# Performance work log

Hardware: AMD Instinct MI355X
Metric: run time of the kernel (lower is better)

## Reference

```python
import jax, jax.numpy as jnp
import numpy as np

T, N = 64, 512
DL, DA, DV = 300, 128, 128
HL, HA, HV = 256, 128, 128
MEM, DF = 256, 128
H_ATT1, H_ATT2, H_G1, H_G2, H_OUT = 512, 512, 512, 512, 256
BETA, M_MOD = 2.0, 3
ATT_IN = (HL + HA + HV) * 2      # cStar dim (windowsize=2)
G_IN = ATT_IN + MEM


def setup_inputs() -> dict:
    key = jax.random.key(0)
    ks = iter(jax.random.split(key, 48))

    def p(*shape):
        return jax.random.normal(next(ks), shape, jnp.float32) * 0.05

    inp = {}
    inp["x"] = jax.random.normal(next(ks), (T, N, DL + DA + DV), jnp.float32)
    for m, (d, h) in (("l", (DL, HL)), ("a", (DA, HA)), ("v", (DV, HV))):
        inp["Wih_" + m] = p(4 * h, d)   # torch LSTMCell weight_ih [4h, d]
        inp["Whh_" + m] = p(4 * h, h)
        inp["bih_" + m] = p(4 * h)
        inp["bhh_" + m] = p(4 * h)
    inp["att1_w1"], inp["att1_b1"] = p(H_ATT1, ATT_IN), p(H_ATT1)
    inp["att1_w2"], inp["att1_b2"] = p(ATT_IN, H_ATT1), p(ATT_IN)
    inp["att2_w1"], inp["att2_b1"] = p(H_ATT2, ATT_IN), p(H_ATT2)
    inp["att2_w2"], inp["att2_b2"] = p(MEM, H_ATT2), p(MEM)
    inp["g1_w1"], inp["g1_b1"] = p(H_G1, G_IN), p(H_G1)
    inp["g1_w2"], inp["g1_b2"] = p(MEM, H_G1), p(MEM)
    inp["g2_w1"], inp["g2_b1"] = p(H_G2, G_IN), p(H_G2)
    inp["g2_w2"], inp["g2_b2"] = p(MEM, H_G2), p(MEM)
    inp["fl_w"], inp["fl_b"] = p(DF, HL), p(DF)
    inp["fa_w"], inp["fa_b"] = p(DF, HA), p(DF)
    inp["fv_w"], inp["fv_b"] = p(DF, HV), p(DF)
    inp["o_w1"], inp["o_b1"] = p(H_OUT, DF + MEM), p(H_OUT)
    inp["o_w2"], inp["o_b2"] = p(1, H_OUT), p(1)
    return inp


def _lin(z, w, b):
    return z @ w.T + b


def _lstm_cell(xt, h, c, Wih, Whh, bih, bhh):
    # torch.nn.LSTMCell: gate order i, f, g, o
    gates = xt @ Wih.T + h @ Whh.T + bih + bhh
    i, f, g, o = jnp.split(gates, 4, axis=1)
    c2 = jax.nn.sigmoid(f) * c + jax.nn.sigmoid(i) * jnp.tanh(g)
    h2 = jax.nn.sigmoid(o) * jnp.tanh(c2)
    return h2, c2


def reference(x, Wih_l, Whh_l, bih_l, bhh_l, Wih_a, Whh_a, bih_a, bhh_a,
              Wih_v, Whh_v, bih_v, bhh_v,
              att1_w1, att1_b1, att1_w2, att1_b2,
              att2_w1, att2_b1, att2_w2, att2_b2,
              g1_w1, g1_b1, g1_w2, g1_b2, g2_w1, g2_b1, g2_w2, g2_b2,
              fl_w, fl_b, fa_w, fa_b, fv_w, fv_b,
              o_w1, o_b1, o_w2, o_b2):
    n = x.shape[1]

    def step(carry, xt):
        h_l, c_l, h_a, c_a, h_v, c_v, mem = carry
        x_l, x_a, x_v = xt[:, :DL], xt[:, DL:DL + DA], xt[:, DL + DA:]
        nh_l, nc_l = _lstm_cell(x_l, h_l, c_l, Wih_l, Whh_l, bih_l, bhh_l)
        nh_a, nc_a = _lstm_cell(x_a, h_a, c_a, Wih_a, Whh_a, bih_a, bhh_a)
        nh_v, nc_v = _lstm_cell(x_v, h_v, c_v, Wih_v, Whh_v, bih_v, bhh_v)
        # cStar = [prev cells, new cells]  -> [n, ATT_IN]
        cStar = jnp.concatenate([c_l, c_a, c_v, nc_l, nc_a, nc_v], axis=1)
        att = jax.nn.softmax(
            _lin(jax.nn.relu(_lin(cStar, att1_w1, att1_b1)), att1_w2, att1_b2),
            axis=1)
        attended = att * cStar
        cHat = jnp.tanh(
            _lin(jax.nn.relu(_lin(attended, att2_w1, att2_b1)), att2_w2, att2_b2))
        both = jnp.concatenate([attended, mem], axis=1)
        gamma1 = jax.nn.sigmoid(
            _lin(jax.nn.relu(_lin(both, g1_w1, g1_b1)), g1_w2, g1_b2))
        gamma2 = jax.nn.sigmoid(
            _lin(jax.nn.relu(_lin(both, g2_w1, g2_b1)), g2_w2, g2_b2))
        mem = gamma1 * mem + gamma2 * cHat
        return (nh_l, nc_l, nh_a, nc_a, nh_v, nc_v, mem), None

    z = lambda d: jnp.zeros((n, d), x.dtype)
    init = (z(HL), z(HL), z(HA), z(HA), z(HV), z(HV), z(MEM))
    (h_l, c_l, h_a, c_a, h_v, c_v, mem), _ = jax.lax.scan(step, init, x)

    def compute_exp(logits):
        return jnp.exp(logits - jnp.max(logits))  # global max, as in source

    p_l = compute_exp(_lin(h_l, fl_w, fl_b))
    p_a = compute_exp(_lin(h_a, fa_w, fa_b))
    p_v = compute_exp(_lin(h_v, fv_w, fv_b))
    e = BETA / (M_MOD - 1)
    lav = (p_l ** e) * jnp.log(p_l) + (p_a ** e) * jnp.log(p_a) + (p_v ** e) * jnp.log(p_v)
    last_hs = jnp.concatenate([lav, mem], axis=1)
    out = _lin(jax.nn.relu(_lin(last_hs, o_w1, o_b1)), o_w2, o_b2)
    return out.flatten()
```

## Files before the change

kernel.cpp:

```cpp
#include <hip/hip_runtime.h>
#include <string.h>

typedef __bf16 bf16_t;
typedef bf16_t bf16x8 __attribute__((ext_vector_type(8)));
typedef bf16_t bf16x4 __attribute__((ext_vector_type(4)));
typedef float  f32x4  __attribute__((ext_vector_type(4)));

#define MFMA16(a,b,c) __builtin_amdgcn_mfma_f32_16x16x32_bf16((a),(b),(c),0,0,0)

#define TSTEPS 64
#define NB     512
#define DIN    556
#define LDSK   40
#define GRIDP  256
#define GXD    33

#define HWREG_XCC_ID (20 | (0 << 6) | ((4 - 1) << 11))

#define OFF_WIHP_L 0u
#define OFF_WHH_L  327680u
#define OFF_WIHP_A 589824u
#define OFF_WHH_A  655360u
#define OFF_WIHP_V 720896u
#define OFF_WHH_V  786432u
#define OFF_ATT1W1 851968u
#define OFF_ATT1W2 1376256u
#define OFF_ATT2W1 1900544u
#define OFF_ATT2W2 2424832u
#define OFF_G1W1   2555904u
#define OFF_G1W2   3211264u
#define OFF_G2W1   3342336u
#define OFF_G2W2   3997696u
#define OFF_FLW    4128768u
#define OFF_FAW    4161536u
#define OFF_FVW    4177920u

__device__ __forceinline__ float sigmoidf_(float x) {
  return 1.0f / (1.0f + __expf(-x));
}
__device__ __forceinline__ float tanhf_(float x) {
  x = fminf(fmaxf(x, -15.0f), 15.0f);
  float e = __expf(2.0f * x);
  return (e - 1.0f) / (e + 1.0f);
}

struct PArgs {
  const float* x;
  const float* bih_l; const float* bhh_l;
  const float* bih_a; const float* bhh_a;
  const float* bih_v; const float* bhh_v;
  const float* att1_b1; const float* att1_b2;
  const float* att2_b1; const float* att2_b2;
  const float* g1_b1; const float* g1_b2;
  const float* g2_b1; const float* g2_b2;
  const float* fl_b; const float* fa_b; const float* fv_b;
  const float* o_w1; const float* o_b1; const float* o_w2; const float* o_b2;
  const float* cvt_src[17];
  unsigned cvt_dst[17];
  int cvt_K[17]; int cvt_Kpad[17]; int cvt_rows[17];
  bf16_t* POOL; bf16_t* XL; bf16_t* XA; bf16_t* XV;
  bf16_t* HB0; bf16_t* HB1; float* CBUF; float* MEMF; bf16_t* MEMBF;
  bf16_t* CSTAR; bf16_t* CSTAR2; bf16_t* Z1; float* LOGB; bf16_t* ATTD; bf16_t* Z3;
  float* PL; float* MAXP; float* BSUM;
  unsigned* BAR;
  float* out;
  int allow_team;
};


__device__ __forceinline__ void gbar(unsigned* bar, unsigned k, int bid) {
  __syncthreads();
  if (threadIdx.x == 0) {
    __threadfence();
    unsigned* gc   = bar + (bid & 7) * 16;
    unsigned* root = bar + 128;
    if (__hip_atomic_fetch_add(gc, 1u, __ATOMIC_ACQ_REL, __HIP_MEMORY_SCOPE_AGENT)
        == 32u * (k + 1u) - 1u) {
      __hip_atomic_fetch_add(root, 1u, __ATOMIC_ACQ_REL, __HIP_MEMORY_SCOPE_AGENT);
    }
    while (__hip_atomic_load(root, __ATOMIC_RELAXED, __HIP_MEMORY_SCOPE_AGENT)
           < 8u * (k + 1u)) {
      __builtin_amdgcn_s_sleep(1);
    }
    __threadfence();
  }
  __syncthreads();
}

__device__ __forceinline__ void lbar(unsigned* ctr, unsigned target) {
  asm volatile("s_waitcnt vmcnt(0)" ::: "memory");
  __syncthreads();
  if (threadIdx.x == 0) {
    __hip_atomic_fetch_add(ctr, 1u, __ATOMIC_RELAXED, __HIP_MEMORY_SCOPE_AGENT);
    while (__hip_atomic_load(ctr, __ATOMIC_RELAXED, __HIP_MEMORY_SCOPE_AGENT)
           < target) {
      __builtin_amdgcn_s_sleep(1);
    }
    asm volatile("buffer_inv\n\ts_waitcnt vmcnt(0)" ::: "memory");
  }
  __syncthreads();
}

__device__ __forceinline__ void gates_body(const PArgs& p, int job, int t, char* SM,
                                           const bf16_t* hbase, bf16_t* houtb,
                                           bf16_t* cstar)
{
  bf16_t* AlB[2] = { (bf16_t*)SM,            (bf16_t*)(SM + 5120) };
  bf16_t* WlB[2] = { (bf16_t*)(SM + 10240),  (bf16_t*)(SM + 20480) };
  float (*Gx)[64][GXD] = (float (*)[64][GXD])SM;

  const int tid = threadIdx.x;
  const int m0 = (job >> 4) * 64;
  const int y  = job & 15;

  const bf16_t *xp, *Wih, *Whh;
  int Kx, Hm, hoff, j0, oldbase, boff;
  if (y < 8) {
    xp = p.XL + (size_t)t * NB * 320; Wih = p.POOL + OFF_WIHP_L; Whh = p.POOL + OFF_WHH_L;
    Kx = 320; Hm = 256; hoff = 0; j0 = y * 32; oldbase = 0; boff = 0;
  } else if (y < 12) {
    xp = p.XA + (size_t)t * NB * 128; Wih = p.POOL + OFF_WIHP_A; Whh = p.POOL + OFF_WHH_A;
    Kx = 128; Hm = 128; hoff = 131072; j0 = (y - 8) * 32; oldbase = 256; boff = 1024;
  } else {
    xp = p.XV + (size_t)t * NB * 128; Wih = p.POOL + OFF_WIHP_V; Whh = p.POOL + OFF_WHH_V;
    Kx = 128; Hm = 128; hoff = 196608; j0 = (y - 12) * 32; oldbase = 384; boff = 1536;
  }

  const int wave = tid >> 6, lane = tid & 63;
  const int lrow = lane & 15, quad = lane >> 4;
  const int srow = tid >> 2, schunk = (tid & 3) * 8;
  const int wrow = tid >> 1, wchunk = (tid & 1) * 16;
  const int g = wrow >> 5, jr = wrow & 31;

  f32x4 acc[4][2];
  #pragma unroll
  for (int mi = 0; mi < 4; mi++)
    #pragma unroll
    for (int ni = 0; ni < 2; ni++) acc[mi][ni] = f32x4{0.f, 0.f, 0.f, 0.f};

  for (int ph = 0; ph < 2; ph++) {
    const bf16_t* Ab; const bf16_t* Wb; int lda_, ldw_, K_;
    if (ph == 0) { Ab = xp;            lda_ = Kx; K_ = Kx; Wb = Wih; ldw_ = Kx; }
    else         { Ab = hbase + hoff;  lda_ = Hm; K_ = Hm; Wb = Whh; ldw_ = Hm; }

    const bf16_t* Arow = Ab + (size_t)(m0 + srow) * lda_ + schunk;
    const bf16_t* Wrow = Wb + (size_t)(g * Hm + j0 + jr) * ldw_ + wchunk;
    const int nI = K_ >> 5;

    bf16x8 av  = *(const bf16x8*)(Arow);
    bf16x8 wv0 = *(const bf16x8*)(Wrow);
    bf16x8 wv1 = *(const bf16x8*)(Wrow + 8);
    *(bf16x8*)(AlB[0] + srow * LDSK + schunk) = av;
    *(bf16x8*)(WlB[0] + wrow * LDSK + wchunk) = wv0;
    *(bf16x8*)(WlB[0] + wrow * LDSK + wchunk + 8) = wv1;

    for (int i = 0; i < nI; i++) {
      const int cur = i & 1;
      const bool more = (i + 1 < nI);
      if (more) {
        av  = *(const bf16x8*)(Arow + (i + 1) * 32);
        wv0 = *(const bf16x8*)(Wrow + (i + 1) * 32);
        wv1 = *(const bf16x8*)(Wrow + (i + 1) * 32 + 8);
      }
      __syncthreads();
      if (more) {
        *(bf16x8*)(AlB[cur ^ 1] + srow * LDSK + schunk) = av;
        *(bf16x8*)(WlB[cur ^ 1] + wrow * LDSK + wchunk) = wv0;
        *(bf16x8*)(WlB[cur ^ 1] + wrow * LDSK + wchunk + 8) = wv1;
      }
      bf16x8 afr[4], bfr[2];
      #pragma unroll
      for (int mi = 0; mi < 4; mi++)
        afr[mi] = *(const bf16x8*)(AlB[cur] + (mi * 16 + lrow) * LDSK + quad * 8);
      #pragma unroll
      for (int ni = 0; ni < 2; ni++)
        bfr[ni] = *(const bf16x8*)(WlB[cur] + (wave * 32 + ni * 16 + lrow) * LDSK + quad * 8);
      #pragma unroll
      for (int mi = 0; mi < 4; mi++)
        #pragma unroll
        for (int ni = 0; ni < 2; ni++)
          acc[mi][ni] = MFMA16(afr[mi], bfr[ni], acc[mi][ni]);
    }
    __syncthreads();
  }

  #pragma unroll
  for (int mi = 0; mi < 4; mi++)
    #pragma unroll
    for (int ni = 0; ni < 2; ni++) {
      int col = ni * 16 + lrow;
      float bv = p.BSUM[boff + wave * Hm + j0 + col];
      #pragma unroll
      for (int r = 0; r < 4; r++) {
        Gx[wave][mi * 16 + quad * 4 + r][col] = acc[mi][ni][r] + bv;
      }
    }
  __syncthreads();

  float* cbuf = p.CBUF + hoff;
  int m = tid >> 2, jb = (tid & 3) * 8;
  #pragma unroll
  for (int i = 0; i < 8; i++) {
    int j = jb + i;
    float gi = Gx[0][m][j], gf = Gx[1][m][j], gg = Gx[2][m][j], go = Gx[3][m][j];
    size_t off = (size_t)(m0 + m) * Hm + (j0 + j);
    float c_old = cbuf[off];
    float c2 = sigmoidf_(gf) * c_old + sigmoidf_(gi) * tanhf_(gg);
    float h2 = sigmoidf_(go) * tanhf_(c2);
    cbuf[off] = c2;
    houtb[hoff + off] = (bf16_t)h2;
    size_t cs = (size_t)(m0 + m) * 1024 + oldbase + (j0 + j);
    cstar[cs] = (bf16_t)c_old;
    cstar[cs + 512] = (bf16_t)c2;
  }
  __syncthreads();
}

__device__ __forceinline__ void lin_body(
    const bf16_t* __restrict__ A, int lda,
    const bf16_t* __restrict__ W, int ldw,
    const float* __restrict__ bias,
    bf16_t* Cb, float* Cf, int ldc, int K, int act,
    int m0, int n0, char* SM)
{
  bf16_t* AlB[2] = { (bf16_t*)SM,            (bf16_t*)(SM + 5120) };
  bf16_t* WlB[2] = { (bf16_t*)(SM + 10240),  (bf16_t*)(SM + 15360) };
  const int tid = threadIdx.x;
  const int wave = tid >> 6, lane = tid & 63;
  const int wm = (wave >> 1) * 32, wn = (wave & 1) * 32;
  const int lrow = lane & 15, quad = lane >> 4;
  const int srow = tid >> 2, schunk = (tid & 3) * 8;

  f32x4 acc[2][2];
  #pragma unroll
  for (int mi = 0; mi < 2; mi++)
    #pragma unroll
    for (int ni = 0; ni < 2; ni++) acc[mi][ni] = f32x4{0.f, 0.f, 0.f, 0.f};

  const bf16_t* Arow = A + (size_t)(m0 + srow) * lda + schunk;
  const bf16_t* Wrow = W + (size_t)(n0 + srow) * ldw + schunk;
  const int nI = K >> 5;

  bf16x8 av = *(const bf16x8*)(Arow);
  bf16x8 wv = *(const bf16x8*)(Wrow);
  *(bf16x8*)(AlB[0] + srow * LDSK + schunk) = av;
  *(bf16x8*)(WlB[0] + srow * LDSK + schunk) = wv;

  for (int i = 0; i < nI; i++) {
    const int cur = i & 1;
    const bool more = (i + 1 < nI);
    if (more) {
      av = *(const bf16x8*)(Arow + (i + 1) * 32);
      wv = *(const bf16x8*)(Wrow + (i + 1) * 32);
    }
    __syncthreads();
    if (more) {
      *(bf16x8*)(AlB[cur ^ 1] + srow * LDSK + schunk) = av;
      *(bf16x8*)(WlB[cur ^ 1] + srow * LDSK + schunk) = wv;
    }
    bf16x8 a0 = *(const bf16x8*)(AlB[cur] + (wm + lrow) * LDSK + quad * 8);
    bf16x8 a1 = *(const bf16x8*)(AlB[cur] + (wm + 16 + lrow) * LDSK + quad * 8);
    bf16x8 b0 = *(const bf16x8*)(WlB[cur] + (wn + lrow) * LDSK + quad * 8);
    bf16x8 b1 = *(const bf16x8*)(WlB[cur] + (wn + 16 + lrow) * LDSK + quad * 8);
    acc[0][0] = MFMA16(a0, b0, acc[0][0]);
    acc[0][1] = MFMA16(a0, b1, acc[0][1]);
    acc[1][0] = MFMA16(a1, b0, acc[1][0]);
    acc[1][1] = MFMA16(a1, b1, acc[1][1]);
  }
  __syncthreads();

  #pragma unroll
  for (int mi = 0; mi < 2; mi++)
    #pragma unroll
    for (int ni = 0; ni < 2; ni++) {
      int row0 = m0 + wm + mi * 16 + quad * 4;
      int col = n0 + wn + ni * 16 + lrow;
      float bv = bias[col];
      #pragma unroll
      for (int r = 0; r < 4; r++) {
        float v = acc[mi][ni][r] + bv;
        if (act == 1) v = fmaxf(v, 0.f);
        size_t off = (size_t)(row0 + r) * ldc + col;
        if (Cb) Cb[off] = (bf16_t)v;
        if (Cf) Cf[off] = v;
      }
    }
}

__device__ __forceinline__ void softmax_body(const PArgs& p, int n, char* SM,
                                             const bf16_t* cstar) {
  float* red = (float*)SM;
  const int tid = threadIdx.x;
  float4 v = *(const float4*)(p.LOGB + (size_t)n * 1024 + tid * 4);
  float mx = fmaxf(fmaxf(v.x, v.y), fmaxf(v.z, v.w));
  red[tid] = mx; __syncthreads();
  for (int s = 128; s > 0; s >>= 1) {
    if (tid < s) red[tid] = fmaxf(red[tid], red[tid + s]);
    __syncthreads();
  }
  mx = red[0]; __syncthreads();
  float e0 = __expf(v.x - mx), e1 = __expf(v.y - mx);
  float e2 = __expf(v.z - mx), e3 = __expf(v.w - mx);
  red[tid] = e0 + e1 + e2 + e3; __syncthreads();
  for (int s = 128; s > 0; s >>= 1) {
    if (tid < s) red[tid] += red[tid + s];
    __syncthreads();
  }
  float inv = 1.0f / red[0];
  bf16x4 c4 = *(const bf16x4*)(cstar + (size_t)n * 1024 + tid * 4);
  bf16x4 o;
  o[0] = (bf16_t)(e0 * inv * (float)c4[0]);
  o[1] = (bf16_t)(e1 * inv * (float)c4[1]);
  o[2] = (bf16_t)(e2 * inv * (float)c4[2]);
  o[3] = (bf16_t)(e3 * inv * (float)c4[3]);
  *(bf16x4*)(p.ATTD + (size_t)n * 1024 + tid * 4) = o;
  __syncthreads();
}

__device__ __forceinline__ void z3_body(const PArgs& p, int job, char* SM) {
  bf16_t* AlB[2] = { (bf16_t*)SM,            (bf16_t*)(SM + 5120) };
  bf16_t* WlB[2] = { (bf16_t*)(SM + 10240),  (bf16_t*)(SM + 15360) };
  const int tid = threadIdx.x;
  const int m0 = (job & 7) * 64, n0 = (job >> 3) * 64;
  const int wave = tid >> 6, lane = tid & 63;
  const int wm = (wave >> 1) * 32, wn = (wave & 1) * 32;
  const int lrow = lane & 15, quad = lane >> 4;
  const int srow = tid >> 2, schunk = (tid & 3) * 8;

  const bf16_t* W; const float* b; int K, nloc;
  if (n0 < 512)       { W = p.POOL + OFF_ATT2W1; b = p.att2_b1; K = 1024; nloc = n0; }
  else if (n0 < 1024) { W = p.POOL + OFF_G1W1;  b = p.g1_b1;  K = 1280; nloc = n0 - 512; }
  else                { W = p.POOL + OFF_G2W1;  b = p.g2_b1;  K = 1280; nloc = n0 - 1024; }

  f32x4 acc[2][2];
  #pragma unroll
  for (int mi = 0; mi < 2; mi++)
    #pragma unroll
    for (int ni = 0; ni < 2; ni++) acc[mi][ni] = f32x4{0.f, 0.f, 0.f, 0.f};

  const bf16_t* Aatt = p.ATTD + (size_t)(m0 + srow) * 1024 + schunk;
  const bf16_t* Amem = p.MEMBF + (size_t)(m0 + srow) * 256 + schunk;
  const bf16_t* Wrow = W + (size_t)(nloc + srow) * K + schunk;
  const int nI = K >> 5;

  bf16x8 av = *(const bf16x8*)(Aatt);
  bf16x8 wv = *(const bf16x8*)(Wrow);
  *(bf16x8*)(AlB[0] + srow * LDSK + schunk) = av;
  *(bf16x8*)(WlB[0] + srow * LDSK + schunk) = wv;

  for (int i = 0; i < nI; i++) {
    const int cur = i & 1;
    const bool more = (i + 1 < nI);
    if (more) {
      int kn = (i + 1) * 32;
      av = (kn < 1024) ? *(const bf16x8*)(Aatt + kn)
                       : *(const bf16x8*)(Amem + (kn - 1024));
      wv = *(const bf16x8*)(Wrow + kn);
    }
    __syncthreads();
    if (more) {
      *(bf16x8*)(AlB[cur ^ 1] + srow * LDSK + schunk) = av;
      *(bf16x8*)(WlB[cur ^ 1] + srow * LDSK + schunk) = wv;
    }
    bf16x8 a0 = *(const bf16x8*)(AlB[cur] + (wm + lrow) * LDSK + quad * 8);
    bf16x8 a1 = *(const bf16x8*)(AlB[cur] + (wm + 16 + lrow) * LDSK + quad * 8);
    bf16x8 b0 = *(const bf16x8*)(WlB[cur] + (wn + lrow) * LDSK + quad * 8);
    bf16x8 b1 = *(const bf16x8*)(WlB[cur] + (wn + 16 + lrow) * LDSK + quad * 8);
    acc[0][0] = MFMA16(a0, b0, acc[0][0]);
    acc[0][1] = MFMA16(a0, b1, acc[0][1]);
    acc[1][0] = MFMA16(a1, b0, acc[1][0]);
    acc[1][1] = MFMA16(a1, b1, acc[1][1]);
  }
  __syncthreads();

  #pragma unroll
  for (int mi = 0; mi < 2; mi++)
    #pragma unroll
    for (int ni = 0; ni < 2; ni++) {
      int row0 = m0 + wm + mi * 16 + quad * 4;
      int cloc = wn + ni * 16 + lrow;
      float bv = b[nloc + cloc];
      #pragma unroll
      for (int r = 0; r < 4; r++) {
        float v = fmaxf(acc[mi][ni][r] + bv, 0.f);
        p.Z3[(size_t)(row0 + r) * 1536 + n0 + cloc] = (bf16_t)v;
      }
    }
}

__device__ __forceinline__ void gmem_body(const PArgs& p, int job, char* SM) {
  const int tid = threadIdx.x;
  const int m0 = (job & 7) * 64, n0 = (job >> 3) * 64;
  const int wave = tid >> 6, lane = tid & 63;
  const int wm = (wave >> 1) * 32, wn = (wave & 1) * 32;
  const int lrow = lane & 15, quad = lane >> 4;
  const int srow = tid >> 2, schunk = (tid & 3) * 8;

  const bf16_t* Ws[3] = { p.POOL + OFF_ATT2W2, p.POOL + OFF_G1W2, p.POOL + OFF_G2W2 };

  f32x4 acc[3][2][2];
  #pragma unroll
  for (int s = 0; s < 3; s++)
    #pragma unroll
    for (int mi = 0; mi < 2; mi++)
      #pragma unroll
      for (int ni = 0; ni < 2; ni++) acc[s][mi][ni] = f32x4{0.f, 0.f, 0.f, 0.f};

  const bf16_t* Arow = p.Z3 + (size_t)(m0 + srow) * 1536 + schunk;
  bf16x8 avv[3], wvv[3];
  #pragma unroll
  for (int s = 0; s < 3; s++) {
    avv[s] = *(const bf16x8*)(Arow + s * 512);
    wvv[s] = *(const bf16x8*)(Ws[s] + (size_t)(n0 + srow) * 512 + schunk);
  }

  for (int k0 = 0; k0 < 512; k0 += 32) {
    #pragma unroll
    for (int s = 0; s < 3; s++) {
      bf16_t* Az = (bf16_t*)(SM + s * 5120);
      bf16_t* Wz = (bf16_t*)(SM + 15360 + s * 5120);
      *(bf16x8*)(Az + srow * LDSK + schunk) = avv[s];
      *(bf16x8*)(Wz + srow * LDSK + schunk) = wvv[s];
    }
    __syncthreads();
    if (k0 + 32 < 512) {
      #pragma unroll
      for (int s = 0; s < 3; s++) {
        avv[s] = *(const bf16x8*)(Arow + s * 512 + k0 + 32);
        wvv[s] = *(const bf16x8*)(Ws[s] + (size_t)(n0 + srow) * 512 + k0 + 32 + schunk);
      }
    }
    #pragma unroll
    for (int s = 0; s < 3; s++) {
      bf16_t* Az = (bf16_t*)(SM + s * 5120);
      bf16_t* Wz = (bf16_t*)(SM + 15360 + s * 5120);
      bf16x8 a0 = *(const bf16x8*)(Az + (wm + lrow) * LDSK + quad * 8);
      bf16x8 a1 = *(const bf16x8*)(Az + (wm + 16 + lrow) * LDSK + quad * 8);
      bf16x8 b0 = *(const bf16x8*)(Wz + (wn + lrow) * LDSK + quad * 8);
      bf16x8 b1 = *(const bf16x8*)(Wz + (wn + 16 + lrow) * LDSK + quad * 8);
      acc[s][0][0] = MFMA16(a0, b0, acc[s][0][0]);
      acc[s][0][1] = MFMA16(a0, b1, acc[s][0][1]);
      acc[s][1][0] = MFMA16(a1, b0, acc[s][1][0]);
      acc[s][1][1] = MFMA16(a1, b1, acc[s][1][1]);
    }
    __syncthreads();
  }
  #pragma unroll
  for (int mi = 0; mi < 2; mi++)
    #pragma unroll
    for (int ni = 0; ni < 2; ni++) {
      int row0 = m0 + wm + mi * 16 + quad * 4;
      int col = n0 + wn + ni * 16 + lrow;
      float bC = p.att2_b2[col], b1v = p.g1_b2[col], b2v = p.g2_b2[col];
      #pragma unroll
      for (int r = 0; r < 4; r++) {
        float cHat = tanhf_(acc[0][mi][ni][r] + bC);
        float g1 = sigmoidf_(acc[1][mi][ni][r] + b1v);
        float g2 = sigmoidf_(acc[2][mi][ni][r] + b2v);
        size_t off = (size_t)(row0 + r) * 256 + col;
        float nm = g1 * p.MEMF[off] + g2 * cHat;
        p.MEMF[off] = nm;
        p.MEMBF[off] = (bf16_t)nm;
      }
    }
}

__device__ __forceinline__ void maxpart_body(const PArgs& p, int job, char* SM) {
  float* red = (float*)SM;
  const int b = job >> 4, chunk = job & 15;
  const int tid = threadIdx.x;
  float mx = -3.4e38f;
  for (int i = tid; i < 32 * 128; i += 256) {
    int n = chunk * 32 + (i >> 7), j = i & 127;
    mx = fmaxf(mx, p.PL[(size_t)n * 384 + b * 128 + j]);
  }
  red[tid] = mx; __syncthreads();
  for (int s = 128; s > 0; s >>= 1) {
    if (tid < s) red[tid] = fmaxf(red[tid], red[tid + s]);
    __syncthreads();
  }
  if (tid == 0) p.MAXP[job] = red[0];
  __syncthreads();
}

__device__ __forceinline__ void out_body(const PArgs& p, int n, char* SM) {
  float* hs  = (float*)SM;
  float* red = (float*)(SM + 1536);
  float* Ms  = (float*)(SM + 2560);
  const int tid = threadIdx.x;
  if (tid < 3) {
    float m = -3.4e38f;
    #pragma unroll
    for (int i = 0; i < 16; i++) m = fmaxf(m, p.MAXP[tid * 16 + i]);
    Ms[tid] = m;
  }
  __syncthreads();
  const float M0 = Ms[0], M1 = Ms[1], M2 = Ms[2];
  for (int idx = tid; idx < 384; idx += 256) {
    float v;
    if (idx < 128) {
      float d0 = p.PL[(size_t)n * 384 + idx] - M0;
      float d1 = p.PL[(size_t)n * 384 + 128 + idx] - M1;
      float d2 = p.PL[(size_t)n * 384 + 256 + idx] - M2;
      v = __expf(d0) * d0 + __expf(d1) * d1 + __expf(d2) * d2;
    } else {
      v = p.MEMF[(size_t)n * 256 + idx - 128];
    }
    hs[idx] = v;
  }
  __syncthreads();
  float acc = p.o_b1[tid];
  const float* wr = p.o_w1 + (size_t)tid * 384;
  #pragma unroll 4
  for (int k = 0; k < 384; k += 4) {
    float4 w = *(const float4*)(wr + k);
    acc += w.x * hs[k] + w.y * hs[k + 1] + w.z * hs[k + 2] + w.w * hs[k + 3];
  }
  red[tid] = fmaxf(acc, 0.f) * p.o_w2[tid];
  __syncthreads();
  for (int s = 128; s > 0; s >>= 1) {
    if (tid < s) red[tid] += red[tid + s];
    __syncthreads();
  }
  if (tid == 0) p.out[n] = red[0] + p.o_b2[0];
  __syncthreads();
}

__device__ __forceinline__ void attn_chain(const PArgs& p, int g, int rb,
                                           const bf16_t* cs_prev, char* SM,
                                           unsigned* teamc, unsigned& tk)
{
  if (rb < 8)
    lin_body(cs_prev, 1024, p.POOL + OFF_ATT1W1, 1024, p.att1_b1,
             p.Z1, (float*)0, 512, 1024, 1, g * 64, rb * 64, SM);
  lbar(teamc, 24u * (++tk));
  if (rb < 16)
    lin_body(p.Z1, 512, p.POOL + OFF_ATT1W2, 512, p.att1_b2,
             (bf16_t*)0, p.LOGB, 1024, 512, 0, g * 64, rb * 64, SM);
  lbar(teamc, 24u * (++tk));
  for (int j = rb; j < 64; j += 24) softmax_body(p, g * 64 + j, SM, cs_prev);
  lbar(teamc, 24u * (++tk));
  z3_body(p, (rb << 3) | g, SM);
  lbar(teamc, 24u * (++tk));
  if (rb < 4) gmem_body(p, (rb << 3) | g, SM);
}

__global__ void __launch_bounds__(256) persist_kernel(PArgs p) {
  __shared__ __align__(16) char SM[34816];
  __shared__ int meta[12];
  const int bid = blockIdx.x;
  const int tid = threadIdx.x;
  unsigned bk = 0;

  {
    float4* z = (float4*)p.HB0;
    for (int i = bid * 256 + tid; i < 180224; i += GRIDP * 256)
      z[i] = make_float4(0.f, 0.f, 0.f, 0.f);

    int gid = bid * 256 + tid;
    if (gid < 1024)      p.BSUM[gid] = p.bih_l[gid] + p.bhh_l[gid];
    else if (gid < 1536) p.BSUM[gid] = p.bih_a[gid - 1024] + p.bhh_a[gid - 1024];
    else if (gid < 2048) p.BSUM[gid] = p.bih_v[gid - 1536] + p.bhh_v[gid - 1536];

    for (int r = bid; r < TSTEPS * NB; r += GRIDP) {
      const float4* xr = (const float4*)(p.x + (size_t)r * DIN);
      int q = tid;
      if (q < 144) {
        float4 v; bf16_t* dst;
        if (q < 80) {
          v = (q < 75) ? xr[q] : make_float4(0.f, 0.f, 0.f, 0.f);
          dst = p.XL + (size_t)r * 320 + q * 4;
        } else if (q < 112) {
          v = xr[75 + (q - 80)];
          dst = p.XA + (size_t)r * 128 + (q - 80) * 4;
        } else {
          v = xr[107 + (q - 112)];
          dst = p.XV + (size_t)r * 128 + (q - 112) * 4;
        }
        bf16x4 o;
        o[0] = (bf16_t)v.x; o[1] = (bf16_t)v.y; o[2] = (bf16_t)v.z; o[3] = (bf16_t)v.w;
        *(bf16x4*)dst = o;
      }
    }

    for (int m = 0; m < 17; m++) {
      const float* src = p.cvt_src[m];
      bf16_t* dst = p.POOL + p.cvt_dst[m];
      int K = p.cvt_K[m], Kp = p.cvt_Kpad[m], R = p.cvt_rows[m];
      int Kq = Kp >> 2, Ksq = K >> 2;
      for (int r = bid; r < R; r += GRIDP) {
        const float4* sr = (const float4*)(src + (size_t)r * K);
        for (int q = tid; q < Kq; q += 256) {
          float4 v = (q < Ksq) ? sr[q] : make_float4(0.f, 0.f, 0.f, 0.f);
          bf16x4 o;
          o[0] = (bf16_t)v.x; o[1] = (bf16_t)v.y; o[2] = (bf16_t)v.z; o[3] = (bf16_t)v.w;
          *(bf16x4*)(dst + (size_t)r * Kp + q * 4) = o;
        }
      }
    }

    if (tid == 0) {
      unsigned raw = __builtin_amdgcn_s_getreg(HWREG_XCC_ID);
      if (raw > 7u) {
        __hip_atomic_store(p.BAR + 159, 1u, __ATOMIC_RELAXED, __HIP_MEMORY_SCOPE_AGENT);
        raw &= 7u;
      }
      meta[0] = (int)raw;
      meta[1] = (int)__hip_atomic_fetch_add(p.BAR + 160 + raw * 16, 1u,
                    __ATOMIC_RELAXED, __HIP_MEMORY_SCOPE_AGENT);
    }
  }
  gbar(p.BAR, bk++, bid);

  if (tid < 8)
    meta[2 + tid] = (int)__hip_atomic_load(p.BAR + 160 + tid * 16,
                        __ATOMIC_RELAXED, __HIP_MEMORY_SCOPE_AGENT);
  if (tid == 8)
    meta[10] = (int)__hip_atomic_load(p.BAR + 159,
                   __ATOMIC_RELAXED, __HIP_MEMORY_SCOPE_AGENT);
  __syncthreads();
  bool teammode = (meta[10] == 0) && (p.allow_team != 0);
  #pragma unroll
  for (int i = 0; i < 8; i++)
    if (meta[2 + i] != 32) teammode = false;

  if (teammode) {
    const int g = meta[0];
    const int rank = meta[1];
    unsigned* fullc = p.BAR + 288 + g * 16;
    unsigned* teamc = p.BAR + 416 + g * 16;
    unsigned lk = 0, tk = 0;
    const int ra = rank - 24;
    const int rb = rank;

    for (int t = 0; t < TSTEPS; t++) {
      lbar(fullc, 32u * (++lk));
      const bf16_t* hin = (t & 1) ? p.HB1 : p.HB0;
      bf16_t* hout      = (t & 1) ? p.HB0 : p.HB1;
      bf16_t* cs_cur    = (t & 1) ? p.CSTAR2 : p.CSTAR;
      const bf16_t* cs_prev = (t & 1) ? p.CSTAR : p.CSTAR2;
      if (ra >= 0) {
        gates_body(p, g * 16 + ra,     t, SM, hin, hout, cs_cur);
        gates_body(p, g * 16 + 8 + ra, t, SM, hin, hout, cs_cur);
      } else if (t > 0) {
        attn_chain(p, g, rb, cs_prev, SM, teamc, tk);
      }
    }
    lbar(fullc, 32u * (++lk));
    if (ra < 0) attn_chain(p, g, rb, p.CSTAR2, SM, teamc, tk);
  } else {
    for (int t = 0; t < TSTEPS; t++) {
      const bf16_t* hin = (t & 1) ? p.HB1 : p.HB0;
      bf16_t* hout      = (t & 1) ? p.HB0 : p.HB1;
      for (int job = bid; job < 128; job += GRIDP)
        gates_body(p, job, t, SM, hin, hout, p.CSTAR);
      gbar(p.BAR, bk++, bid);

      for (int job = bid; job < 64; job += GRIDP)
        lin_body(p.CSTAR, 1024, p.POOL + OFF_ATT1W1, 1024, p.att1_b1,
                 p.Z1, (float*)0, 512, 1024, 1, (job & 7) * 64, (job >> 3) * 64, SM);
      gbar(p.BAR, bk++, bid);

      for (int job = bid; job < 128; job += GRIDP)
        lin_body(p.Z1, 512, p.POOL + OFF_ATT1W2, 512, p.att1_b2,
                 (bf16_t*)0, p.LOGB, 1024, 512, 0, (job & 7) * 64, (job >> 3) * 64, SM);
      gbar(p.BAR, bk++, bid);

      for (int job = bid; job < 512; job += GRIDP)
        softmax_body(p, job, SM, p.CSTAR);
      gbar(p.BAR, bk++, bid);

      for (int job = bid; job < 192; job += GRIDP) z3_body(p, job, SM);
      gbar(p.BAR, bk++, bid);

      for (int job = bid; job < 32; job += GRIDP) gmem_body(p, job, SM);
      gbar(p.BAR, bk++, bid);
    }
  }
  gbar(p.BAR, bk++, bid);

  for (int job = bid; job < 48; job += GRIDP) {
    int mat = job >> 4, rem = job & 15;
    int m0 = (rem & 7) * 64, n0 = (rem >> 3) * 64;
    const bf16_t* h = (mat == 0) ? p.HB0 : (mat == 1) ? p.HB0 + 131072 : p.HB0 + 196608;
    int lda = (mat == 0) ? 256 : 128;
    const bf16_t* W = p.POOL + ((mat == 0) ? OFF_FLW : (mat == 1) ? OFF_FAW : OFF_FVW);
    const float* b = (mat == 0) ? p.fl_b : (mat == 1) ? p.fa_b : p.fv_b;
    lin_body(h, lda, W, lda, b, (bf16_t*)0, p.PL + mat * 128, 384, lda, 0, m0, n0, SM);
  }
  gbar(p.BAR, bk++, bid);

  for (int job = bid; job < 48; job += GRIDP) maxpart_body(p, job, SM);
  gbar(p.BAR, bk++, bid);

  for (int job = bid; job < 512; job += GRIDP) out_body(p, job, SM);
}


__global__ __launch_bounds__(256) void zero_kernel(float4* p, int n4) {
  int i = blockIdx.x * 256 + threadIdx.x;
  if (i < n4) p[i] = make_float4(0.f, 0.f, 0.f, 0.f);
}

__global__ __launch_bounds__(256) void cvt_pad_kernel(
    const float* __restrict__ src, bf16_t* __restrict__ dst, int K, int Kpad)
{
  int r = blockIdx.x;
  for (int k = threadIdx.x; k < Kpad; k += 256)
    dst[(size_t)r * Kpad + k] = (k < K) ? (bf16_t)src[(size_t)r * K + k] : (bf16_t)0.f;
}

__global__ __launch_bounds__(256) void cvt_x_kernel(
    const float* __restrict__ x, bf16_t* __restrict__ xl,
    bf16_t* __restrict__ xa, bf16_t* __restrict__ xv)
{
  int r = blockIdx.x;
  const float* xr = x + (size_t)r * DIN;
  for (int c = threadIdx.x; c < 576; c += 256) {
    if (c < 320) {
      xl[(size_t)r * 320 + c] = (c < 300) ? (bf16_t)xr[c] : (bf16_t)0.f;
    } else if (c < 448) {
      xa[(size_t)r * 128 + (c - 320)] = (bf16_t)xr[300 + (c - 320)];
    } else {
      xv[(size_t)r * 128 + (c - 448)] = (bf16_t)xr[428 + (c - 448)];
    }
  }
}

__global__ __launch_bounds__(256) void bias_sum_kernel(
    const float* __restrict__ bih_l, const float* __restrict__ bhh_l,
    const float* __restrict__ bih_a, const float* __restrict__ bhh_a,
    const float* __restrict__ bih_v, const float* __restrict__ bhh_v,
    float* __restrict__ bsum)
{
  int i = blockIdx.x * 256 + threadIdx.x;
  if (i < 1024)      bsum[i] = bih_l[i] + bhh_l[i];
  else if (i < 1536) bsum[i] = bih_a[i - 1024] + bhh_a[i - 1024];
  else if (i < 2048) bsum[i] = bih_v[i - 1536] + bhh_v[i - 1536];
}

__global__ __launch_bounds__(256) void gates_cell_kernel_fb(PArgs p, int t) {
  __shared__ __align__(16) char SM[34816];
  const bf16_t* hin = (t & 1) ? p.HB1 : p.HB0;
  bf16_t* hout      = (t & 1) ? p.HB0 : p.HB1;
  gates_body(p, blockIdx.x * 16 + blockIdx.y, t, SM, hin, hout, p.CSTAR);
}

__global__ __launch_bounds__(256) void mfma_lin_kernel_fb(
    const bf16_t* A, int lda, const bf16_t* W, int ldw,
    const float* bias, bf16_t* Cb, float* Cf, int ldc, int K, int act)
{
  __shared__ __align__(16) char SM[20480];
  lin_body(A, lda, W, ldw, bias, Cb, Cf, ldc, K, act,
           blockIdx.x * 64, blockIdx.y * 64, SM);
}

__global__ __launch_bounds__(256) void softmax_attend_kernel_fb(PArgs p) {
  __shared__ __align__(16) char SM[1024];
  softmax_body(p, blockIdx.x, SM, p.CSTAR);
}

__global__ __launch_bounds__(256) void z3_kernel_fb(PArgs p) {
  __shared__ __align__(16) char SM[20480];
  z3_body(p, blockIdx.x + blockIdx.y * 8, SM);
}

__global__ __launch_bounds__(256) void gmem_kernel_fb(PArgs p) {
  __shared__ __align__(16) char SM[30720];
  gmem_body(p, blockIdx.x + blockIdx.y * 8, SM);
}

__global__ __launch_bounds__(256) void maxpart_kernel_fb(PArgs p) {
  __shared__ __align__(16) char SM[1024];
  maxpart_body(p, blockIdx.x, SM);
}

__global__ __launch_bounds__(256) void out_kernel_fb(PArgs p) {
  __shared__ __align__(16) char SM[2576];
  out_body(p, blockIdx.x, SM);
}

extern "C" void kernel_launch(void* const* d_in, const int* in_sizes, int n_in,
                              void* d_out, int out_size, void* d_ws, size_t ws_size,
                              hipStream_t stream)
{
  const float* x      = (const float*)d_in[0];
  const float* Wih_l  = (const float*)d_in[1];
  const float* Whh_l  = (const float*)d_in[2];
  const float* bih_l  = (const float*)d_in[3];
  const float* bhh_l  = (const float*)d_in[4];
  const float* Wih_a  = (const float*)d_in[5];
  const float* Whh_a  = (const float*)d_in[6];
  const float* bih_a  = (const float*)d_in[7];
  const float* bhh_a  = (const float*)d_in[8];
  const float* Wih_v  = (const float*)d_in[9];
  const float* Whh_v  = (const float*)d_in[10];
  const float* bih_v  = (const float*)d_in[11];
  const float* bhh_v  = (const float*)d_in[12];
  const float* att1_w1 = (const float*)d_in[13];
  const float* att1_b1 = (const float*)d_in[14];
  const float* att1_w2 = (const float*)d_in[15];
  const float* att1_b2 = (const float*)d_in[16];
  const float* att2_w1 = (const float*)d_in[17];
  const float* att2_b1 = (const float*)d_in[18];
  const float* att2_w2 = (const float*)d_in[19];
  const float* att2_b2 = (const float*)d_in[20];
  const float* g1_w1  = (const float*)d_in[21];
  const float* g1_b1  = (const float*)d_in[22];
  const float* g1_w2  = (const float*)d_in[23];
  const float* g1_b2  = (const float*)d_in[24];
  const float* g2_w1  = (const float*)d_in[25];
  const float* g2_b1  = (const float*)d_in[26];
  const float* g2_w2  = (const float*)d_in[27];
  const float* g2_b2  = (const float*)d_in[28];
  const float* fl_w   = (const float*)d_in[29];
  const float* fl_b   = (const float*)d_in[30];
  const float* fa_w   = (const float*)d_in[31];
  const float* fa_b   = (const float*)d_in[32];
  const float* fv_w   = (const float*)d_in[33];
  const float* fv_b   = (const float*)d_in[34];
  const float* o_w1   = (const float*)d_in[35];
  const float* o_b1   = (const float*)d_in[36];
  const float* o_w2   = (const float*)d_in[37];
  const float* o_b2   = (const float*)d_in[38];

  char* base = (char*)d_ws;
  PArgs pa;
  pa.x = x;
  pa.bih_l = bih_l; pa.bhh_l = bhh_l;
  pa.bih_a = bih_a; pa.bhh_a = bhh_a;
  pa.bih_v = bih_v; pa.bhh_v = bhh_v;
  pa.att1_b1 = att1_b1; pa.att1_b2 = att1_b2;
  pa.att2_b1 = att2_b1; pa.att2_b2 = att2_b2;
  pa.g1_b1 = g1_b1; pa.g1_b2 = g1_b2;
  pa.g2_b1 = g2_b1; pa.g2_b2 = g2_b2;
  pa.fl_b = fl_b; pa.fa_b = fa_b; pa.fv_b = fv_b;
  pa.o_w1 = o_w1; pa.o_b1 = o_b1; pa.o_w2 = o_w2; pa.o_b2 = o_b2;

  const float* csrc[17] = { Wih_l, Whh_l, Wih_a, Whh_a, Wih_v, Whh_v,
                            att1_w1, att1_w2, att2_w1, att2_w2,
                            g1_w1, g1_w2, g2_w1, g2_w2, fl_w, fa_w, fv_w };
  const unsigned cdst[17] = { OFF_WIHP_L, OFF_WHH_L, OFF_WIHP_A, OFF_WHH_A,
                              OFF_WIHP_V, OFF_WHH_V, OFF_ATT1W1, OFF_ATT1W2,
                              OFF_ATT2W1, OFF_ATT2W2, OFF_G1W1, OFF_G1W2,
                              OFF_G2W1, OFF_G2W2, OFF_FLW, OFF_FAW, OFF_FVW };
  const int cK[17]   = { 300, 256, 128, 128, 128, 128, 1024, 512, 1024, 512,
                         1280, 512, 1280, 512, 256, 128, 128 };
  const int cKp[17]  = { 320, 256, 128, 128, 128, 128, 1024, 512, 1024, 512,
                         1280, 512, 1280, 512, 256, 128, 128 };
  const int cR[17]   = { 1024, 1024, 512, 512, 512, 512, 512, 1024, 512, 256,
                         512, 256, 512, 256, 128, 128, 128 };
  for (int i = 0; i < 17; i++) {
    pa.cvt_src[i] = csrc[i]; pa.cvt_dst[i] = cdst[i];
    pa.cvt_K[i] = cK[i]; pa.cvt_Kpad[i] = cKp[i]; pa.cvt_rows[i] = cR[i];
  }

  pa.POOL   = (bf16_t*)(base);
  pa.XL     = (bf16_t*)(base + 8388608);
  pa.XA     = (bf16_t*)(base + 29360128);
  pa.XV     = (bf16_t*)(base + 37748736);
  pa.HB0    = (bf16_t*)(base + 46137344);
  pa.HB1    = (bf16_t*)(base + 46661632);
  pa.CBUF   = (float*) (base + 47185920);
  pa.MEMF   = (float*) (base + 48234496);
  pa.MEMBF  = (bf16_t*)(base + 48758784);
  pa.CSTAR  = (bf16_t*)(base + 49020928);
  pa.Z1     = (bf16_t*)(base + 50069504);
  pa.LOGB   = (float*) (base + 50593792);
  pa.ATTD   = (bf16_t*)(base + 52690944);
  pa.Z3     = (bf16_t*)(base + 53739520);
  pa.PL     = (float*) (base + 55312384);
  pa.MAXP   = (float*) (base + 56098816);
  pa.BSUM   = (float*) (base + 56099072);
  pa.BAR    = (unsigned*)(base + 56107264);
  pa.CSTAR2 = (bf16_t*)(base + 56111616);
  pa.out    = (float*)d_out;
  pa.allow_team = (ws_size >= 57160192u) ? 1 : 0;

  hipMemsetAsync(pa.BAR, 0, 4096, stream);

  void* kargs[] = { (void*)&pa };
  hipError_t e = hipLaunchCooperativeKernel((const void*)persist_kernel,
                                            dim3(GRIDP), dim3(256), kargs, 0, stream);
  if (e == hipSuccess) return;

  zero_kernel<<<704, 256, 0, stream>>>((float4*)pa.HB0, 180224);
  cvt_x_kernel<<<TSTEPS * NB, 256, 0, stream>>>(x, pa.XL, pa.XA, pa.XV);
  for (int i = 0; i < 17; i++)
    cvt_pad_kernel<<<cR[i], 256, 0, stream>>>(csrc[i], pa.POOL + cdst[i], cK[i], cKp[i]);
  bias_sum_kernel<<<8, 256, 0, stream>>>(bih_l, bhh_l, bih_a, bhh_a, bih_v, bhh_v, pa.BSUM);

  for (int t = 0; t < TSTEPS; t++) {
    gates_cell_kernel_fb<<<dim3(8, 16), 256, 0, stream>>>(pa, t);
    mfma_lin_kernel_fb<<<dim3(8, 8), 256, 0, stream>>>(
        pa.CSTAR, 1024, pa.POOL + OFF_ATT1W1, 1024, att1_b1,
        pa.Z1, (float*)nullptr, 512, 1024, 1);
    mfma_lin_kernel_fb<<<dim3(8, 16), 256, 0, stream>>>(
        pa.Z1, 512, pa.POOL + OFF_ATT1W2, 512, att1_b2,
        (bf16_t*)nullptr, pa.LOGB, 1024, 512, 0);
    softmax_attend_kernel_fb<<<512, 256, 0, stream>>>(pa);
    z3_kernel_fb<<<dim3(8, 24), 256, 0, stream>>>(pa);
    gmem_kernel_fb<<<dim3(8, 4), 256, 0, stream>>>(pa);
  }

  bf16_t* h_l = pa.HB0;
  bf16_t* h_a = pa.HB0 + 131072;
  bf16_t* h_v = pa.HB0 + 196608;
  mfma_lin_kernel_fb<<<dim3(8, 2), 256, 0, stream>>>(
      h_l, 256, pa.POOL + OFF_FLW, 256, fl_b, (bf16_t*)nullptr, pa.PL, 384, 256, 0);
  mfma_lin_kernel_fb<<<dim3(8, 2), 256, 0, stream>>>(
      h_a, 128, pa.POOL + OFF_FAW, 128, fa_b, (bf16_t*)nullptr, pa.PL + 128, 384, 128, 0);
  mfma_lin_kernel_fb<<<dim3(8, 2), 256, 0, stream>>>(
      h_v, 128, pa.POOL + OFF_FVW, 128, fv_b, (bf16_t*)nullptr, pa.PL + 256, 384, 128, 0);
  maxpart_kernel_fb<<<48, 256, 0, stream>>>(pa);
  out_kernel_fb<<<512, 256, 0, stream>>>(pa);
}
```

Baseline: 4.449 ms.

## Fuse softmax-attend into z3 GEMM prologue, removing a barrier stage

The separate softmax/attend pass that wrote ATTD is removed. Each z3 block now computes row max and sum over LOGB itself, then builds the attended bf16 operand on the fly while loading its A tile. This drops one grid/team barrier per timestep and the ATTD global round trip. In exchange, each of the 24 column-block jobs recomputes the row softmax statistics and the exps redundantly, and the barrier counter offsets are moved.

```diff
diff --git a/kernel.cpp b/kernel.cpp
--- a/kernel.cpp
+++ b/kernel.cpp
@@ -60,7 +60,7 @@
   int cvt_K[17]; int cvt_Kpad[17]; int cvt_rows[17];
   bf16_t* POOL; bf16_t* XL; bf16_t* XA; bf16_t* XV;
   bf16_t* HB0; bf16_t* HB1; float* CBUF; float* MEMF; bf16_t* MEMBF;
-  bf16_t* CSTAR; bf16_t* CSTAR2; bf16_t* Z1; float* LOGB; bf16_t* ATTD; bf16_t* Z3;
+  bf16_t* CSTAR; bf16_t* CSTAR2; bf16_t* Z1; float* LOGB; bf16_t* Z3;
   float* PL; float* MAXP; float* BSUM;
   unsigned* BAR;
   float* out;
@@ -287,39 +287,12 @@
     }
 }
 
-__device__ __forceinline__ void softmax_body(const PArgs& p, int n, char* SM,
-                                             const bf16_t* cstar) {
-  float* red = (float*)SM;
-  const int tid = threadIdx.x;
-  float4 v = *(const float4*)(p.LOGB + (size_t)n * 1024 + tid * 4);
-  float mx = fmaxf(fmaxf(v.x, v.y), fmaxf(v.z, v.w));
-  red[tid] = mx; __syncthreads();
-  for (int s = 128; s > 0; s >>= 1) {
-    if (tid < s) red[tid] = fmaxf(red[tid], red[tid + s]);
-    __syncthreads();
-  }
-  mx = red[0]; __syncthreads();
-  float e0 = __expf(v.x - mx), e1 = __expf(v.y - mx);
-  float e2 = __expf(v.z - mx), e3 = __expf(v.w - mx);
-  red[tid] = e0 + e1 + e2 + e3; __syncthreads();
-  for (int s = 128; s > 0; s >>= 1) {
-    if (tid < s) red[tid] += red[tid + s];
-    __syncthreads();
-  }
-  float inv = 1.0f / red[0];
-  bf16x4 c4 = *(const bf16x4*)(cstar + (size_t)n * 1024 + tid * 4);
-  bf16x4 o;
-  o[0] = (bf16_t)(e0 * inv * (float)c4[0]);
-  o[1] = (bf16_t)(e1 * inv * (float)c4[1]);
-  o[2] = (bf16_t)(e2 * inv * (float)c4[2]);
-  o[3] = (bf16_t)(e3 * inv * (float)c4[3]);
-  *(bf16x4*)(p.ATTD + (size_t)n * 1024 + tid * 4) = o;
-  __syncthreads();
-}
-
-__device__ __forceinline__ void z3_body(const PArgs& p, int job, char* SM) {
+__device__ __forceinline__ void z3_body(const PArgs& p, int job,
+                                        const bf16_t* __restrict__ cstar,
+                                        char* SM) {
   bf16_t* AlB[2] = { (bf16_t*)SM,            (bf16_t*)(SM + 5120) };
   bf16_t* WlB[2] = { (bf16_t*)(SM + 10240),  (bf16_t*)(SM + 15360) };
+  float*  part   = (float*)(SM + 20480);
   const int tid = threadIdx.x;
   const int m0 = (job & 7) * 64, n0 = (job >> 3) * 64;
   const int wave = tid >> 6, lane = tid & 63;
@@ -327,6 +300,32 @@
   const int lrow = lane & 15, quad = lane >> 4;
   const int srow = tid >> 2, schunk = (tid & 3) * 8;
 
+  const int seg = tid & 3;
+  const float* lrowp = p.LOGB + (size_t)(m0 + srow) * 1024 + seg * 256;
+  float mrow = -3.4e38f;
+  #pragma unroll 4
+  for (int q = 0; q < 64; q++) {
+    float4 v = ((const float4*)lrowp)[q];
+    mrow = fmaxf(mrow, fmaxf(fmaxf(v.x, v.y), fmaxf(v.z, v.w)));
+  }
+  part[srow * 4 + seg] = mrow;
+  __syncthreads();
+  mrow = fmaxf(fmaxf(part[srow * 4 + 0], part[srow * 4 + 1]),
+               fmaxf(part[srow * 4 + 2], part[srow * 4 + 3]));
+  float ssum = 0.f;
+  #pragma unroll 4
+  for (int q = 0; q < 64; q++) {
+    float4 v = ((const float4*)lrowp)[q];
+    ssum += __expf(v.x - mrow) + __expf(v.y - mrow)
+          + __expf(v.z - mrow) + __expf(v.w - mrow);
+  }
+  __syncthreads();
+  part[srow * 4 + seg] = ssum;
+  __syncthreads();
+  const float invr = 1.0f / (part[srow * 4 + 0] + part[srow * 4 + 1] +
+                             part[srow * 4 + 2] + part[srow * 4 + 3]);
+  const float mxr = mrow;
+
   const bf16_t* W; const float* b; int K, nloc;
   if (n0 < 512)       { W = p.POOL + OFF_ATT2W1; b = p.att2_b1; K = 1024; nloc = n0; }
   else if (n0 < 1024) { W = p.POOL + OFF_G1W1;  b = p.g1_b1;  K = 1280; nloc = n0 - 512; }
@@ -338,28 +337,53 @@
     #pragma unroll
     for (int ni = 0; ni < 2; ni++) acc[mi][ni] = f32x4{0.f, 0.f, 0.f, 0.f};
 
-  const bf16_t* Aatt = p.ATTD + (size_t)(m0 + srow) * 1024 + schunk;
+  const float*  Alog = p.LOGB + (size_t)(m0 + srow) * 1024 + schunk;
+  const bf16_t* Acs  = cstar + (size_t)(m0 + srow) * 1024 + schunk;
   const bf16_t* Amem = p.MEMBF + (size_t)(m0 + srow) * 256 + schunk;
   const bf16_t* Wrow = W + (size_t)(nloc + srow) * K + schunk;
   const int nI = K >> 5;
 
-  bf16x8 av = *(const bf16x8*)(Aatt);
+  float4 l0, l1; bf16x8 c8; bf16x8 mv; bool frommem;
+  auto fetch = [&](int kk) {
+    if (kk < 1024) {
+      l0 = *(const float4*)(Alog + kk);
+      l1 = *(const float4*)(Alog + kk + 4);
+      c8 = *(const bf16x8*)(Acs + kk);
+      frommem = false;
+    } else {
+      mv = *(const bf16x8*)(Amem + (kk - 1024));
+      frommem = true;
+    }
+  };
+  auto pack = [&]() -> bf16x8 {
+    if (frommem) return mv;
+    bf16x8 o;
+    o[0] = (bf16_t)(__expf(l0.x - mxr) * invr * (float)c8[0]);
+    o[1] = (bf16_t)(__expf(l0.y - mxr) * invr * (float)c8[1]);
+    o[2] = (bf16_t)(__expf(l0.z - mxr) * invr * (float)c8[2]);
+    o[3] = (bf16_t)(__expf(l0.w - mxr) * invr * (float)c8[3]);
+    o[4] = (bf16_t)(__expf(l1.x - mxr) * invr * (float)c8[4]);
+    o[5] = (bf16_t)(__expf(l1.y - mxr) * invr * (float)c8[5]);
+    o[6] = (bf16_t)(__expf(l1.z - mxr) * invr * (float)c8[6]);
+    o[7] = (bf16_t)(__expf(l1.w - mxr) * invr * (float)c8[7]);
+    return o;
+  };
+
+  fetch(0);
   bf16x8 wv = *(const bf16x8*)(Wrow);
-  *(bf16x8*)(AlB[0] + srow * LDSK + schunk) = av;
+  *(bf16x8*)(AlB[0] + srow * LDSK + schunk) = pack();
   *(bf16x8*)(WlB[0] + srow * LDSK + schunk) = wv;
 
   for (int i = 0; i < nI; i++) {
     const int cur = i & 1;
     const bool more = (i + 1 < nI);
     if (more) {
-      int kn = (i + 1) * 32;
-      av = (kn < 1024) ? *(const bf16x8*)(Aatt + kn)
-                       : *(const bf16x8*)(Amem + (kn - 1024));
-      wv = *(const bf16x8*)(Wrow + kn);
+      fetch((i + 1) * 32);
+      wv = *(const bf16x8*)(Wrow + (i + 1) * 32);
     }
     __syncthreads();
     if (more) {
-      *(bf16x8*)(AlB[cur ^ 1] + srow * LDSK + schunk) = av;
+      *(bf16x8*)(AlB[cur ^ 1] + srow * LDSK + schunk) = pack();
       *(bf16x8*)(WlB[cur ^ 1] + srow * LDSK + schunk) = wv;
     }
     bf16x8 a0 = *(const bf16x8*)(AlB[cur] + (wm + lrow) * LDSK + quad * 8);
@@ -538,9 +562,7 @@
     lin_body(p.Z1, 512, p.POOL + OFF_ATT1W2, 512, p.att1_b2,
              (bf16_t*)0, p.LOGB, 1024, 512, 0, g * 64, rb * 64, SM);
   lbar(teamc, 24u * (++tk));
-  for (int j = rb; j < 64; j += 24) softmax_body(p, g * 64 + j, SM, cs_prev);
-  lbar(teamc, 24u * (++tk));
-  z3_body(p, (rb << 3) | g, SM);
+  z3_body(p, (rb << 3) | g, cs_prev, SM);
   lbar(teamc, 24u * (++tk));
   if (rb < 4) gmem_body(p, (rb << 3) | g, SM);
 }
@@ -627,8 +649,8 @@
   if (teammode) {
     const int g = meta[0];
     const int rank = meta[1];
-    unsigned* fullc = p.BAR + 288 + g * 16;
-    unsigned* teamc = p.BAR + 416 + g * 16;
+    unsigned* fullc = p.BAR + 512 + g * 64;
+    unsigned* teamc = p.BAR + 512 + g * 64 + 32;
     unsigned lk = 0, tk = 0;
     const int ra = rank - 24;
     const int rb = rank;
@@ -666,11 +688,8 @@
                  (bf16_t*)0, p.LOGB, 1024, 512, 0, (job & 7) * 64, (job >> 3) * 64, SM);
       gbar(p.BAR, bk++, bid);
 
-      for (int job = bid; job < 512; job += GRIDP)
-        softmax_body(p, job, SM, p.CSTAR);
-      gbar(p.BAR, bk++, bid);
-
-      for (int job = bid; job < 192; job += GRIDP) z3_body(p, job, SM);
+      for (int job = bid; job < 192; job += GRIDP)
+        z3_body(p, job, p.CSTAR, SM);
       gbar(p.BAR, bk++, bid);
 
       for (int job = bid; job < 32; job += GRIDP) gmem_body(p, job, SM);
@@ -755,14 +774,9 @@
            blockIdx.x * 64, blockIdx.y * 64, SM);
 }
 
-__global__ __launch_bounds__(256) void softmax_attend_kernel_fb(PArgs p) {
-  __shared__ __align__(16) char SM[1024];
-  softmax_body(p, blockIdx.x, SM, p.CSTAR);
-}
-
 __global__ __launch_bounds__(256) void z3_kernel_fb(PArgs p) {
-  __shared__ __align__(16) char SM[20480];
-  z3_body(p, blockIdx.x + blockIdx.y * 8, SM);
+  __shared__ __align__(16) char SM[21504];
+  z3_body(p, blockIdx.x + blockIdx.y * 8, p.CSTAR, SM);
 }
 
 __global__ __launch_bounds__(256) void gmem_kernel_fb(PArgs p) {
@@ -867,7 +881,6 @@
   pa.CSTAR  = (bf16_t*)(base + 49020928);
   pa.Z1     = (bf16_t*)(base + 50069504);
   pa.LOGB   = (float*) (base + 50593792);
-  pa.ATTD   = (bf16_t*)(base + 52690944);
   pa.Z3     = (bf16_t*)(base + 53739520);
   pa.PL     = (float*) (base + 55312384);
   pa.MAXP   = (float*) (base + 56098816);
@@ -898,7 +911,6 @@
     mfma_lin_kernel_fb<<<dim3(8, 16), 256, 0, stream>>>(
         pa.Z1, 512, pa.POOL + OFF_ATT1W2, 512, att1_b2,
         (bf16_t*)nullptr, pa.LOGB, 1024, 512, 0);
-    softmax_attend_kernel_fb<<<512, 256, 0, stream>>>(pa);
     z3_kernel_fb<<<dim3(8, 24), 256, 0, stream>>>(pa);
     gmem_kernel_fb<<<dim3(8, 4), 256, 0, stream>>>(pa);
   }
```

New measurement: 6.200 ms. +39.3%, slower.
